# Kernel optimization log

Hardware: AMD Instinct MI355X
Metric: run time of the kernel (lower is better)

The kernel has to match this reference:

```python
import jax, jax.numpy as jnp
import numpy as np

EPS = 1e-5

def _layernorm(x):
    mu = jnp.mean(x, axis=-1, keepdims=True)
    var = jnp.mean((x - mu) ** 2, axis=-1, keepdims=True)
    return (x - mu) / jnp.sqrt(var + EPS)

def _mlp_silu_ln(h, w0, b0, w1, b1):
    z = jnp.maximum(h @ w0 + b0, 0.0) @ w1 + b1
    z = z * jax.nn.sigmoid(z)  # SiLU
    return _layernorm(z)

def _scatter_mean(msgs, tgt, n_nodes):
    s = jax.ops.segment_sum(msgs, tgt, num_segments=n_nodes)
    cnt = jax.ops.segment_sum(jnp.ones((msgs.shape[0],), msgs.dtype), tgt, num_segments=n_nodes)
    return jnp.where(cnt[:, None] > 0, s / jnp.maximum(cnt, 1.0)[:, None], 0.0)

def setup_inputs() -> dict:
    key = jax.random.key(0)
    ks = jax.random.split(key, 6)
    N, E, D_IN, D = 100000, 600000, 64, 128
    s = 0.1
    return {
        "x": jax.random.normal(ks[0], (N, D_IN), jnp.float32),
        "edge_index": jax.random.randint(ks[1], (2, E), 0, N, jnp.int64),
        "ie_w0": jax.random.normal(ks[2], (D_IN, D), jnp.float32) * s,
        "ie_b0": jnp.zeros((D,), jnp.float32),
        "ie_w1": jax.random.normal(ks[3], (D, D), jnp.float32) * s,
        "ie_b1": jnp.zeros((D,), jnp.float32),
        "lw0": jax.random.normal(ks[4], (3, D, D), jnp.float32) * s,
        "lb0": jnp.zeros((3, D), jnp.float32),
        "lw1": jax.random.normal(ks[5], (3, D, D), jnp.float32) * s,
        "lb1": jnp.zeros((3, D), jnp.float32),
    }

def reference(x, edge_index, ie_w0, ie_b0, ie_w1, ie_b1, lw0, lb0, lw1, lb1):
    n_nodes = x.shape[0]
    src, tgt = edge_index[0], edge_index[1]
    # initial embedding: MLP(relu) -> SiLU -> LayerNorm
    h = _mlp_silu_ln(x, ie_w0, ie_b0, ie_w1, ie_b1)

    def step(h, params):
        w0, b0, w1, b1 = params
        z = _mlp_silu_ln(h, w0, b0, w1, b1)
        agg = _scatter_mean(z[src], tgt, n_nodes)  # mean aggregation over incoming edges
        return agg + h, None  # residual

    h, _ = jax.lax.scan(step, h, (lw0, lb0, lw1, lb1))
    return h
```

## Files before the change

kernel.cpp:

```cpp
#include <hip/hip_runtime.h>

typedef short short8 __attribute__((ext_vector_type(8)));
typedef float f32x4 __attribute__((ext_vector_type(4)));

union V16 { uint4 u; unsigned short s[8]; short8 v; };

#define CAP 48

__device__ __forceinline__ unsigned short f2bf(float f) {
  unsigned u = __builtin_bit_cast(unsigned, f);
  u += 0x7fffu + ((u >> 16) & 1u);
  return (unsigned short)(u >> 16);
}
__device__ __forceinline__ float bf2f(unsigned short b) {
  unsigned u = ((unsigned)b) << 16;
  return __builtin_bit_cast(float, u);
}
__device__ __forceinline__ unsigned cvtpk(float lo, float hi) {
  unsigned r;
  asm("v_cvt_pk_bf16_f32 %0, %1, %2" : "=v"(r) : "v"(lo), "v"(hi));
  return r;
}

__device__ __forceinline__ void tcast_one(const float* __restrict__ w,
                                          uint4* __restrict__ wf, int K, int idx) {
  int NF64 = (K / 4) * 64;
  int b = idx / NF64;
  int r = idx - b * NF64;
  int f = r >> 6;
  int l = r & 63;
  int KB = K / 32;
  int n0 = f / KB;
  int k0 = f - n0 * KB;
  int n = n0 * 16 + (l & 15);
  int ks = k0 * 32 + (l >> 4) * 8;
  const float* src = w + (size_t)b * K * 128 + (size_t)ks * 128 + n;
  V16 o;
#pragma unroll
  for (int j = 0; j < 8; j++) o.s[j] = f2bf(src[j * 128]);
  wf[idx] = o.u;
}

__global__ __launch_bounds__(512) void prep_kernel(
    const float* __restrict__ ie_w0, uint4* __restrict__ w0f_ie,
    const float* __restrict__ ie_w1, uint4* __restrict__ w1f_ie,
    const float* __restrict__ lw0, uint4* __restrict__ w0f_l,
    const float* __restrict__ lw1, uint4* __restrict__ w1f_l,
    uint4* __restrict__ cursor4, int nc4,
    const int* __restrict__ ei, int samples, int* __restrict__ flag) {
  int t = blockIdx.x * 512 + threadIdx.x;
  if (t < 1024) { tcast_one(ie_w0, w0f_ie, 64, t); return; }
  t -= 1024;
  if (t < 2048) { tcast_one(ie_w1, w1f_ie, 128, t); return; }
  t -= 2048;
  if (t < 6144) { tcast_one(lw0, w0f_l, 128, t); return; }
  t -= 6144;
  if (t < 6144) { tcast_one(lw1, w1f_l, 128, t); return; }
  t -= 6144;
  if (t < nc4) { uint4 z; z.x = 0; z.y = 0; z.z = 0; z.w = 0; cursor4[t] = z; return; }
  t -= nc4;
  if (t < samples && (t & 1) && ei[t] != 0) atomicOr(flag, 1);
}

__global__ void fill_kernel(const int* __restrict__ ei, const int* __restrict__ flag,
                            int* __restrict__ cursor, int* __restrict__ elist, int E) {
  int e = blockIdx.x * 256 + threadIdx.x;
  if (e >= E) return;
  int f = *flag;
  int s = f ? ei[e] : ei[(size_t)e * 2];
  int t = f ? ei[(size_t)E + e] : ei[((size_t)E + e) * 2];
  int p = atomicAdd(&cursor[t], 1);
  if (p < CAP) elist[t * CAP + p] = s;
}

template <int K, bool OUTBF>
__device__ __forceinline__ void mlp_body(
    const float* __restrict__ in, const uint4* __restrict__ w0f,
    const float* __restrict__ b0, const uint4* __restrict__ w1f,
    const float* __restrict__ b1, float* __restrict__ outF,
    unsigned short* __restrict__ outB, int N, int ntiles,
    uint4* wl, float* bl, int tid) {
  constexpr int KB = K / 32;
  constexpr int NF0 = KB * 8;
  constexpr int TOT = (NF0 + 32) * 64;
  const int lane = tid & 63, wv = tid >> 6;

#pragma unroll
  for (int k = 0; k < TOT / 512; k++) {
    const int i = tid + k * 512;
    const uint4* src = (i < NF0 * 64) ? (w0f + i) : (w1f + (i - NF0 * 64));
    __builtin_amdgcn_global_load_lds(
        (const __attribute__((address_space(1))) void*)src,
        (__attribute__((address_space(3))) void*)(wl + (wv * 64 + k * 512)),
        16, 0, 0);
  }
  if (tid < 128) { bl[tid] = b0[tid]; bl[128 + tid] = b1[tid]; }
  __syncthreads();

  const int c = lane & 15;
  const int q = lane >> 4;
  const int sA = c + 32 * (q & 1);

  for (int tile = blockIdx.x; tile < ntiles; tile += gridDim.x) {
    const int r = tile * 128 + wv * 16 + c;

    short8 afr[KB];
    if (r < N) {
      const float* rp = in + (size_t)r * K + q * 8;
#pragma unroll
      for (int k0 = 0; k0 < KB; k0++) {
        float4 a = *(const float4*)(rp + k0 * 32);
        float4 b = *(const float4*)(rp + k0 * 32 + 4);
        V16 o;
        o.u.x = cvtpk(a.x, a.y); o.u.y = cvtpk(a.z, a.w);
        o.u.z = cvtpk(b.x, b.y); o.u.w = cvtpk(b.z, b.w);
        afr[k0] = o.v;
      }
    } else {
#pragma unroll
      for (int k0 = 0; k0 < KB; k0++) {
        V16 o; o.u.x = 0; o.u.y = 0; o.u.z = 0; o.u.w = 0; afr[k0] = o.v;
      }
    }

    f32x4 acc[8];
#pragma unroll
    for (int n0 = 0; n0 < 8; n0++) {
      acc[n0] = (f32x4){0.f, 0.f, 0.f, 0.f};
#pragma unroll
      for (int k0 = 0; k0 < KB; k0++) {
        V16 w; w.u = wl[(n0 * KB + k0) * 64 + lane];
        acc[n0] = __builtin_amdgcn_mfma_f32_16x16x32_bf16(w.v, afr[k0], acc[n0], 0, 0, 0);
      }
    }

    unsigned pk[8][2];
#pragma unroll
    for (int n0 = 0; n0 < 8; n0++) {
      f32x4 bb = *(const f32x4*)&bl[n0 * 16 + 4 * q];
      float t0 = acc[n0][0] + bb[0]; t0 = t0 > 0.f ? t0 : 0.f;
      float t1 = acc[n0][1] + bb[1]; t1 = t1 > 0.f ? t1 : 0.f;
      float t2 = acc[n0][2] + bb[2]; t2 = t2 > 0.f ? t2 : 0.f;
      float t3 = acc[n0][3] + bb[3]; t3 = t3 > 0.f ? t3 : 0.f;
      pk[n0][0] = cvtpk(t0, t1);
      pk[n0][1] = cvtpk(t2, t3);
    }

    short8 b2[4];
#pragma unroll
    for (int k0 = 0; k0 < 4; k0++) {
      V16 t;
#pragma unroll
      for (int p = 0; p < 4; p++) {
        int src = sA + 16 * (p >> 1);
        unsigned lo = __shfl(pk[2 * k0][p & 1], src, 64);
        unsigned hi = __shfl(pk[2 * k0 + 1][p & 1], src, 64);
        (&t.u.x)[p] = (q & 2) ? hi : lo;
      }
      b2[k0] = t.v;
    }

    f32x4 z[8];
#pragma unroll
    for (int n0 = 0; n0 < 8; n0++) {
      z[n0] = (f32x4){0.f, 0.f, 0.f, 0.f};
#pragma unroll
      for (int k0 = 0; k0 < 4; k0++) {
        V16 w; w.u = wl[NF0 * 64 + (n0 * 4 + k0) * 64 + lane];
        z[n0] = __builtin_amdgcn_mfma_f32_16x16x32_bf16(w.v, b2[k0], z[n0], 0, 0, 0);
      }
    }

    float sum = 0.f, sq = 0.f;
#pragma unroll
    for (int n0 = 0; n0 < 8; n0++) {
      f32x4 bb = *(const f32x4*)&bl[128 + n0 * 16 + 4 * q];
#pragma unroll
      for (int j = 0; j < 4; j++) {
        float v = z[n0][j] + bb[j];
        float sg = v / (1.f + __expf(-v));
        z[n0][j] = sg;
        sum += sg;
        sq += sg * sg;
      }
    }
    sum += __shfl_xor(sum, 16, 64);
    sum += __shfl_xor(sum, 32, 64);
    sq += __shfl_xor(sq, 16, 64);
    sq += __shfl_xor(sq, 32, 64);
    float mu = sum * (1.f / 128.f);
    float rs = rsqrtf(sq * (1.f / 128.f) - mu * mu + 1e-5f);

    if (r < N) {
#pragma unroll
      for (int n0 = 0; n0 < 8; n0++) {
        float v0 = (z[n0][0] - mu) * rs, v1 = (z[n0][1] - mu) * rs;
        float v2 = (z[n0][2] - mu) * rs, v3 = (z[n0][3] - mu) * rs;
        size_t o = (size_t)r * 128 + n0 * 16 + 4 * q;
        if (OUTBF) {
          uint2 st; st.x = cvtpk(v0, v1); st.y = cvtpk(v2, v3);
          *(uint2*)(outB + o) = st;
        } else {
          float4 st; st.x = v0; st.y = v1; st.z = v2; st.w = v3;
          *(float4*)(outF + o) = st;
        }
      }
    }
  }
}

__global__ __launch_bounds__(512, 4) void mlp64_kernel(
    const float* __restrict__ x, const uint4* __restrict__ w0f,
    const float* __restrict__ b0, const uint4* __restrict__ w1f,
    const float* __restrict__ b1, float* __restrict__ h0, int N, int ntiles) {
  __shared__ uint4 wl[48 * 64];
  __shared__ float bl[256];
  mlp_body<64, false>(x, w0f, b0, w1f, b1, h0, nullptr, N, ntiles,
                      wl, bl, threadIdx.x);
}

__global__ __launch_bounds__(512, 4) void mlp128_kernel(
    const float* __restrict__ in, const uint4* __restrict__ w0f,
    const float* __restrict__ b0, const uint4* __restrict__ w1f,
    const float* __restrict__ b1, unsigned short* __restrict__ outB,
    int N, int ntiles) {
  __shared__ uint4 wl[64 * 64];
  __shared__ float bl[256];
  mlp_body<128, true>(in, w0f, b0, w1f, b1, nullptr, outB, N, ntiles,
                      wl, bl, threadIdx.x);
}

__global__ __launch_bounds__(256) void gather_kernel(
    const unsigned short* __restrict__ z, const int* __restrict__ elist,
    const int* __restrict__ cursor, float* __restrict__ h, int N) {
  int t = blockIdx.x * 256 + threadIdx.x;
  int g = t >> 4;
  if (g >= N) return;
  int lane = threadIdx.x & 63;
  int gb = lane & 48;
  int sub = lane & 15;
  int c = sub * 8;
  int o = g * CAP;
  int n = cursor[g];
  n = n < CAP ? n : CAP;
  float* hp = h + (size_t)g * 128 + c;
  float4 h0 = *(const float4*)hp, h1 = *(const float4*)(hp + 4);
  float acc[8] = {0.f, 0.f, 0.f, 0.f, 0.f, 0.f, 0.f, 0.f};
  for (int base = 0; base < n; base += 16) {
    int m = n - base;
    m = m < 16 ? m : 16;
    int sidx = (sub < m) ? elist[o + base + sub] : 0;
    int i = 0;
    for (; i + 4 <= m; i += 4) {
      int s0 = __shfl(sidx, gb + i, 64);
      int s1 = __shfl(sidx, gb + i + 1, 64);
      int s2 = __shfl(sidx, gb + i + 2, 64);
      int s3 = __shfl(sidx, gb + i + 3, 64);
      V16 v0, v1, v2, v3;
      v0.u = *(const uint4*)(z + (size_t)s0 * 128 + c);
      v1.u = *(const uint4*)(z + (size_t)s1 * 128 + c);
      v2.u = *(const uint4*)(z + (size_t)s2 * 128 + c);
      v3.u = *(const uint4*)(z + (size_t)s3 * 128 + c);
#pragma unroll
      for (int j = 0; j < 8; j++)
        acc[j] += (bf2f(v0.s[j]) + bf2f(v1.s[j])) + (bf2f(v2.s[j]) + bf2f(v3.s[j]));
    }
    for (; i < m; i++) {
      int s0 = __shfl(sidx, gb + i, 64);
      V16 v0;
      v0.u = *(const uint4*)(z + (size_t)s0 * 128 + c);
#pragma unroll
      for (int j = 0; j < 8; j++) acc[j] += bf2f(v0.s[j]);
    }
  }
  float inv = n > 0 ? 1.f / (float)n : 0.f;
  h0.x += acc[0] * inv; h0.y += acc[1] * inv; h0.z += acc[2] * inv; h0.w += acc[3] * inv;
  h1.x += acc[4] * inv; h1.y += acc[5] * inv; h1.z += acc[6] * inv; h1.w += acc[7] * inv;
  *(float4*)hp = h0;
  *(float4*)(hp + 4) = h1;
}

extern "C" void kernel_launch(void* const* d_in, const int* in_sizes, int n_in,
                              void* d_out, int out_size, void* d_ws, size_t ws_size,
                              hipStream_t stream) {
  const float* x = (const float*)d_in[0];
  const int* ei = (const int*)d_in[1];
  const float* ie_w0 = (const float*)d_in[2];
  const float* ie_b0 = (const float*)d_in[3];
  const float* ie_w1 = (const float*)d_in[4];
  const float* ie_b1 = (const float*)d_in[5];
  const float* lw0 = (const float*)d_in[6];
  const float* lb0 = (const float*)d_in[7];
  const float* lw1 = (const float*)d_in[8];
  const float* lb1 = (const float*)d_in[9];
  const int N = in_sizes[0] / 64;
  const int E = in_sizes[1] / 2;
  float* h = (float*)d_out;

  char* ws = (char*)d_ws;
  size_t off_b = 0;
  auto carve = [&](size_t bytes) { void* p = ws + off_b; off_b = (off_b + bytes + 255) & ~(size_t)255; return p; };
  unsigned short* zbuf = (unsigned short*)carve((size_t)N * 128 * 2);
  int* elist = (int*)carve((size_t)N * CAP * 4);
  int* flag = (int*)carve(256);
  int* cursor = (int*)carve((size_t)N * 4 + 16);
  uint4* w0f_ie = (uint4*)carve(16 * 64 * 16);
  uint4* w1f_ie = (uint4*)carve(32 * 64 * 16);
  uint4* w0f_l = (uint4*)carve(3 * 32 * 64 * 16);
  uint4* w1f_l = (uint4*)carve(3 * 32 * 64 * 16);

  const int ntiles = (N + 127) / 128;
  const int mgrid = ntiles < 512 ? ntiles : 512;
  const int nc4 = (N + 3) / 4;
  int samples = 2 * E < 8192 ? 2 * E : 8192;

  hipMemsetAsync(flag, 0, 4, stream);
  prep_kernel<<<(15360 + nc4 + samples + 511) / 512, 512, 0, stream>>>(
      ie_w0, w0f_ie, ie_w1, w1f_ie, lw0, w0f_l, lw1, w1f_l,
      (uint4*)cursor, nc4, ei, samples, flag);

  fill_kernel<<<(E + 255) / 256, 256, 0, stream>>>(ei, flag, cursor, elist, E);

  mlp64_kernel<<<mgrid, 512, 0, stream>>>(
      x, w0f_ie, ie_b0, w1f_ie, ie_b1, h, N, ntiles);

  for (int l = 0; l < 3; l++) {
    mlp128_kernel<<<mgrid, 512, 0, stream>>>(
        h, w0f_l + (size_t)l * 32 * 64, lb0 + (size_t)l * 128,
        w1f_l + (size_t)l * 32 * 64, lb1 + (size_t)l * 128, zbuf, N, ntiles);
    gather_kernel<<<((size_t)N * 16 + 255) / 256, 256, 0, stream>>>(
        zbuf, elist, cursor, h, N);
  }
}
```

Measured before the change: 252.4 us.

## Fuse gather-mean residual update with next layer MLP into one kernel

Adds a gmlp kernel that performs the mean aggregation plus residual for layer l, writes h, and immediately runs layer l+1's MLP on the updated row held in registers. The z buffer is now double-buffered so reads and writes can happen in the same kernel. This removes two kernel launches and one round trip of h through global memory per fused layer. In exchange each of the 16 lanes per row handles a whole row's gather serially inside the 512-thread MLP tiling, so there is less parallelism for hiding the latency of the irregular gather loads.

```diff
diff --git a/kernel.cpp b/kernel.cpp
--- a/kernel.cpp
+++ b/kernel.cpp
@@ -74,6 +74,117 @@
 }
 
 template <int K, bool OUTBF>
+__device__ __forceinline__ void mlp_core(
+    const short8 afr[K / 32], const uint4* wl, const float* bl,
+    float* __restrict__ outF, unsigned short* __restrict__ outB,
+    int r, int N, int lane) {
+  constexpr int KB = K / 32;
+  constexpr int NF0 = KB * 8;
+  const int q = lane >> 4;
+  const int c = lane & 15;
+  const int sA = c + 32 * (q & 1);
+
+  f32x4 acc[8];
+#pragma unroll
+  for (int n0 = 0; n0 < 8; n0++) {
+    acc[n0] = (f32x4){0.f, 0.f, 0.f, 0.f};
+#pragma unroll
+    for (int k0 = 0; k0 < KB; k0++) {
+      V16 w; w.u = wl[(n0 * KB + k0) * 64 + lane];
+      acc[n0] = __builtin_amdgcn_mfma_f32_16x16x32_bf16(w.v, afr[k0], acc[n0], 0, 0, 0);
+    }
+  }
+
+  unsigned pk[8][2];
+#pragma unroll
+  for (int n0 = 0; n0 < 8; n0++) {
+    f32x4 bb = *(const f32x4*)&bl[n0 * 16 + 4 * q];
+    float t0 = acc[n0][0] + bb[0]; t0 = t0 > 0.f ? t0 : 0.f;
+    float t1 = acc[n0][1] + bb[1]; t1 = t1 > 0.f ? t1 : 0.f;
+    float t2 = acc[n0][2] + bb[2]; t2 = t2 > 0.f ? t2 : 0.f;
+    float t3 = acc[n0][3] + bb[3]; t3 = t3 > 0.f ? t3 : 0.f;
+    pk[n0][0] = cvtpk(t0, t1);
+    pk[n0][1] = cvtpk(t2, t3);
+  }
+
+  short8 b2[4];
+#pragma unroll
+  for (int k0 = 0; k0 < 4; k0++) {
+    V16 t;
+#pragma unroll
+    for (int p = 0; p < 4; p++) {
+      int src = sA + 16 * (p >> 1);
+      unsigned lo = __shfl(pk[2 * k0][p & 1], src, 64);
+      unsigned hi = __shfl(pk[2 * k0 + 1][p & 1], src, 64);
+      (&t.u.x)[p] = (q & 2) ? hi : lo;
+    }
+    b2[k0] = t.v;
+  }
+
+  f32x4 z[8];
+#pragma unroll
+  for (int n0 = 0; n0 < 8; n0++) {
+    z[n0] = (f32x4){0.f, 0.f, 0.f, 0.f};
+#pragma unroll
+    for (int k0 = 0; k0 < 4; k0++) {
+      V16 w; w.u = wl[NF0 * 64 + (n0 * 4 + k0) * 64 + lane];
+      z[n0] = __builtin_amdgcn_mfma_f32_16x16x32_bf16(w.v, b2[k0], z[n0], 0, 0, 0);
+    }
+  }
+
+  float sum = 0.f, sq = 0.f;
+#pragma unroll
+  for (int n0 = 0; n0 < 8; n0++) {
+    f32x4 bb = *(const f32x4*)&bl[128 + n0 * 16 + 4 * q];
+#pragma unroll
+    for (int j = 0; j < 4; j++) {
+      float v = z[n0][j] + bb[j];
+      float sg = v / (1.f + __expf(-v));
+      z[n0][j] = sg;
+      sum += sg;
+      sq += sg * sg;
+    }
+  }
+  sum += __shfl_xor(sum, 16, 64);
+  sum += __shfl_xor(sum, 32, 64);
+  sq += __shfl_xor(sq, 16, 64);
+  sq += __shfl_xor(sq, 32, 64);
+  float mu = sum * (1.f / 128.f);
+  float rs = rsqrtf(sq * (1.f / 128.f) - mu * mu + 1e-5f);
+
+  if (r < N) {
+#pragma unroll
+    for (int n0 = 0; n0 < 8; n0++) {
+      float v0 = (z[n0][0] - mu) * rs, v1 = (z[n0][1] - mu) * rs;
+      float v2 = (z[n0][2] - mu) * rs, v3 = (z[n0][3] - mu) * rs;
+      size_t o = (size_t)r * 128 + n0 * 16 + 4 * q;
+      if (OUTBF) {
+        uint2 st; st.x = cvtpk(v0, v1); st.y = cvtpk(v2, v3);
+        *(uint2*)(outB + o) = st;
+      } else {
+        float4 st; st.x = v0; st.y = v1; st.z = v2; st.w = v3;
+        *(float4*)(outF + o) = st;
+      }
+    }
+  }
+}
+
+template <int TOT, int NF0>
+__device__ __forceinline__ void stage_weights(const uint4* __restrict__ w0f,
+                                              const uint4* __restrict__ w1f,
+                                              uint4* wl, int tid, int wv) {
+#pragma unroll
+  for (int k = 0; k < TOT / 512; k++) {
+    const int i = tid + k * 512;
+    const uint4* src = (i < NF0 * 64) ? (w0f + i) : (w1f + (i - NF0 * 64));
+    __builtin_amdgcn_global_load_lds(
+        (const __attribute__((address_space(1))) void*)src,
+        (__attribute__((address_space(3))) void*)(wl + (wv * 64 + k * 512)),
+        16, 0, 0);
+  }
+}
+
+template <int K, bool OUTBF>
 __device__ __forceinline__ void mlp_body(
     const float* __restrict__ in, const uint4* __restrict__ w0f,
     const float* __restrict__ b0, const uint4* __restrict__ w1f,
@@ -82,28 +193,16 @@
     uint4* wl, float* bl, int tid) {
   constexpr int KB = K / 32;
   constexpr int NF0 = KB * 8;
-  constexpr int TOT = (NF0 + 32) * 64;
   const int lane = tid & 63, wv = tid >> 6;
-
-#pragma unroll
-  for (int k = 0; k < TOT / 512; k++) {
-    const int i = tid + k * 512;
-    const uint4* src = (i < NF0 * 64) ? (w0f + i) : (w1f + (i - NF0 * 64));
-    __builtin_amdgcn_global_load_lds(
-        (const __attribute__((address_space(1))) void*)src,
-        (__attribute__((address_space(3))) void*)(wl + (wv * 64 + k * 512)),
-        16, 0, 0);
-  }
+  stage_weights<(NF0 + 32) * 64, NF0>(w0f, w1f, wl, tid, wv);
   if (tid < 128) { bl[tid] = b0[tid]; bl[128 + tid] = b1[tid]; }
   __syncthreads();
 
   const int c = lane & 15;
   const int q = lane >> 4;
-  const int sA = c + 32 * (q & 1);
 
   for (int tile = blockIdx.x; tile < ntiles; tile += gridDim.x) {
     const int r = tile * 128 + wv * 16 + c;
-
     short8 afr[KB];
     if (r < N) {
       const float* rp = in + (size_t)r * K + q * 8;
@@ -122,90 +221,7 @@
         V16 o; o.u.x = 0; o.u.y = 0; o.u.z = 0; o.u.w = 0; afr[k0] = o.v;
       }
     }
-
-    f32x4 acc[8];
-#pragma unroll
-    for (int n0 = 0; n0 < 8; n0++) {
-      acc[n0] = (f32x4){0.f, 0.f, 0.f, 0.f};
-#pragma unroll
-      for (int k0 = 0; k0 < KB; k0++) {
-        V16 w; w.u = wl[(n0 * KB + k0) * 64 + lane];
-        acc[n0] = __builtin_amdgcn_mfma_f32_16x16x32_bf16(w.v, afr[k0], acc[n0], 0, 0, 0);
-      }
-    }
-
-    unsigned pk[8][2];
-#pragma unroll
-    for (int n0 = 0; n0 < 8; n0++) {
-      f32x4 bb = *(const f32x4*)&bl[n0 * 16 + 4 * q];
-      float t0 = acc[n0][0] + bb[0]; t0 = t0 > 0.f ? t0 : 0.f;
-      float t1 = acc[n0][1] + bb[1]; t1 = t1 > 0.f ? t1 : 0.f;
-      float t2 = acc[n0][2] + bb[2]; t2 = t2 > 0.f ? t2 : 0.f;
-      float t3 = acc[n0][3] + bb[3]; t3 = t3 > 0.f ? t3 : 0.f;
-      pk[n0][0] = cvtpk(t0, t1);
-      pk[n0][1] = cvtpk(t2, t3);
-    }
-
-    short8 b2[4];
-#pragma unroll
-    for (int k0 = 0; k0 < 4; k0++) {
-      V16 t;
-#pragma unroll
-      for (int p = 0; p < 4; p++) {
-        int src = sA + 16 * (p >> 1);
-        unsigned lo = __shfl(pk[2 * k0][p & 1], src, 64);
-        unsigned hi = __shfl(pk[2 * k0 + 1][p & 1], src, 64);
-        (&t.u.x)[p] = (q & 2) ? hi : lo;
-      }
-      b2[k0] = t.v;
-    }
-
-    f32x4 z[8];
-#pragma unroll
-    for (int n0 = 0; n0 < 8; n0++) {
-      z[n0] = (f32x4){0.f, 0.f, 0.f, 0.f};
-#pragma unroll
-      for (int k0 = 0; k0 < 4; k0++) {
-        V16 w; w.u = wl[NF0 * 64 + (n0 * 4 + k0) * 64 + lane];
-        z[n0] = __builtin_amdgcn_mfma_f32_16x16x32_bf16(w.v, b2[k0], z[n0], 0, 0, 0);
-      }
-    }
-
-    float sum = 0.f, sq = 0.f;
-#pragma unroll
-    for (int n0 = 0; n0 < 8; n0++) {
-      f32x4 bb = *(const f32x4*)&bl[128 + n0 * 16 + 4 * q];
-#pragma unroll
-      for (int j = 0; j < 4; j++) {
-        float v = z[n0][j] + bb[j];
-        float sg = v / (1.f + __expf(-v));
-        z[n0][j] = sg;
-        sum += sg;
-        sq += sg * sg;
-      }
-    }
-    sum += __shfl_xor(sum, 16, 64);
-    sum += __shfl_xor(sum, 32, 64);
-    sq += __shfl_xor(sq, 16, 64);
-    sq += __shfl_xor(sq, 32, 64);
-    float mu = sum * (1.f / 128.f);
-    float rs = rsqrtf(sq * (1.f / 128.f) - mu * mu + 1e-5f);
-
-    if (r < N) {
-#pragma unroll
-      for (int n0 = 0; n0 < 8; n0++) {
-        float v0 = (z[n0][0] - mu) * rs, v1 = (z[n0][1] - mu) * rs;
-        float v2 = (z[n0][2] - mu) * rs, v3 = (z[n0][3] - mu) * rs;
-        size_t o = (size_t)r * 128 + n0 * 16 + 4 * q;
-        if (OUTBF) {
-          uint2 st; st.x = cvtpk(v0, v1); st.y = cvtpk(v2, v3);
-          *(uint2*)(outB + o) = st;
-        } else {
-          float4 st; st.x = v0; st.y = v1; st.z = v2; st.w = v3;
-          *(float4*)(outF + o) = st;
-        }
-      }
-    }
+    mlp_core<K, OUTBF>(afr, wl, bl, outF, outB, r, N, lane);
   }
 }
 
@@ -228,6 +244,107 @@
   __shared__ float bl[256];
   mlp_body<128, true>(in, w0f, b0, w1f, b1, nullptr, outB, N, ntiles,
                       wl, bl, threadIdx.x);
+}
+
+__global__ __launch_bounds__(512) void gmlp_kernel(
+    const unsigned short* __restrict__ zin, const int* __restrict__ elist,
+    const int* __restrict__ cursor, float* __restrict__ h,
+    const uint4* __restrict__ w0f, const float* __restrict__ b0,
+    const uint4* __restrict__ w1f, const float* __restrict__ b1,
+    unsigned short* __restrict__ zout, int N, int ntiles) {
+  __shared__ uint4 wl[64 * 64];
+  __shared__ float bl[256];
+  const int tid = threadIdx.x, lane = tid & 63, wv = tid >> 6;
+  stage_weights<64 * 64, 32>(w0f, w1f, wl, tid, wv);
+  if (tid < 128) { bl[tid] = b0[tid]; bl[128 + tid] = b1[tid]; }
+  __syncthreads();
+
+  const int c = lane & 15;
+  const int q = lane >> 4;
+
+  for (int tile = blockIdx.x; tile < ntiles; tile += gridDim.x) {
+    const int r = tile * 128 + wv * 16 + c;
+    float hv[4][8];
+    if (r < N) {
+      const float* hp = h + (size_t)r * 128 + q * 8;
+      float4 ha[4], hb[4];
+#pragma unroll
+      for (int k0 = 0; k0 < 4; k0++) {
+        ha[k0] = *(const float4*)(hp + k0 * 32);
+        hb[k0] = *(const float4*)(hp + k0 * 32 + 4);
+      }
+      int n = cursor[r];
+      n = n < CAP ? n : CAP;
+      const int o = r * CAP;
+      float acc[4][8];
+#pragma unroll
+      for (int k0 = 0; k0 < 4; k0++)
+#pragma unroll
+        for (int j = 0; j < 8; j++) acc[k0][j] = 0.f;
+      const unsigned short* zq = zin + q * 8;
+      int i = 0;
+      for (; i + 2 <= n; i += 2) {
+        int s0 = elist[o + i], s1 = elist[o + i + 1];
+        V16 u0[4], u1[4];
+#pragma unroll
+        for (int k0 = 0; k0 < 4; k0++) {
+          u0[k0].u = *(const uint4*)(zq + (size_t)s0 * 128 + k0 * 32);
+          u1[k0].u = *(const uint4*)(zq + (size_t)s1 * 128 + k0 * 32);
+        }
+#pragma unroll
+        for (int k0 = 0; k0 < 4; k0++)
+#pragma unroll
+          for (int j = 0; j < 8; j++)
+            acc[k0][j] += bf2f(u0[k0].s[j]) + bf2f(u1[k0].s[j]);
+      }
+      if (i < n) {
+        int s0 = elist[o + i];
+        V16 u0[4];
+#pragma unroll
+        for (int k0 = 0; k0 < 4; k0++)
+          u0[k0].u = *(const uint4*)(zq + (size_t)s0 * 128 + k0 * 32);
+#pragma unroll
+        for (int k0 = 0; k0 < 4; k0++)
+#pragma unroll
+          for (int j = 0; j < 8; j++) acc[k0][j] += bf2f(u0[k0].s[j]);
+      }
+      float inv = n > 0 ? 1.f / (float)n : 0.f;
+      float* hw = h + (size_t)r * 128 + q * 8;
+#pragma unroll
+      for (int k0 = 0; k0 < 4; k0++) {
+        hv[k0][0] = ha[k0].x + acc[k0][0] * inv;
+        hv[k0][1] = ha[k0].y + acc[k0][1] * inv;
+        hv[k0][2] = ha[k0].z + acc[k0][2] * inv;
+        hv[k0][3] = ha[k0].w + acc[k0][3] * inv;
+        hv[k0][4] = hb[k0].x + acc[k0][4] * inv;
+        hv[k0][5] = hb[k0].y + acc[k0][5] * inv;
+        hv[k0][6] = hb[k0].z + acc[k0][6] * inv;
+        hv[k0][7] = hb[k0].w + acc[k0][7] * inv;
+        float4 s0, s1;
+        s0.x = hv[k0][0]; s0.y = hv[k0][1]; s0.z = hv[k0][2]; s0.w = hv[k0][3];
+        s1.x = hv[k0][4]; s1.y = hv[k0][5]; s1.z = hv[k0][6]; s1.w = hv[k0][7];
+        *(float4*)(hw + k0 * 32) = s0;
+        *(float4*)(hw + k0 * 32 + 4) = s1;
+      }
+    } else {
+#pragma unroll
+      for (int k0 = 0; k0 < 4; k0++)
+#pragma unroll
+        for (int j = 0; j < 8; j++) hv[k0][j] = 0.f;
+    }
+
+    short8 afr[4];
+#pragma unroll
+    for (int k0 = 0; k0 < 4; k0++) {
+      V16 o;
+      o.u.x = cvtpk(hv[k0][0], hv[k0][1]);
+      o.u.y = cvtpk(hv[k0][2], hv[k0][3]);
+      o.u.z = cvtpk(hv[k0][4], hv[k0][5]);
+      o.u.w = cvtpk(hv[k0][6], hv[k0][7]);
+      afr[k0] = o.v;
+    }
+    mlp_core<128, true>(afr, wl, bl, nullptr, zout, r, N, lane);
+  }
 }
 
 __global__ __launch_bounds__(256) void gather_kernel(
@@ -300,7 +417,8 @@
   char* ws = (char*)d_ws;
   size_t off_b = 0;
   auto carve = [&](size_t bytes) { void* p = ws + off_b; off_b = (off_b + bytes + 255) & ~(size_t)255; return p; };
-  unsigned short* zbuf = (unsigned short*)carve((size_t)N * 128 * 2);
+  unsigned short* zbufA = (unsigned short*)carve((size_t)N * 128 * 2);
+  unsigned short* zbufB = (unsigned short*)carve((size_t)N * 128 * 2);
   int* elist = (int*)carve((size_t)N * CAP * 4);
   int* flag = (int*)carve(256);
   int* cursor = (int*)carve((size_t)N * 4 + 16);
@@ -324,11 +442,19 @@
   mlp64_kernel<<<mgrid, 512, 0, stream>>>(
       x, w0f_ie, ie_b0, w1f_ie, ie_b1, h, N, ntiles);
 
-  for (int l = 0; l < 3; l++) {
-    mlp128_kernel<<<mgrid, 512, 0, stream>>>(
-        h, w0f_l + (size_t)l * 32 * 64, lb0 + (size_t)l * 128,
-        w1f_l + (size_t)l * 32 * 64, lb1 + (size_t)l * 128, zbuf, N, ntiles);
-    gather_kernel<<<((size_t)N * 16 + 255) / 256, 256, 0, stream>>>(
-        zbuf, elist, cursor, h, N);
-  }
-}
+  mlp128_kernel<<<mgrid, 512, 0, stream>>>(
+      h, w0f_l, lb0, w1f_l, lb1, zbufA, N, ntiles);
+
+  gmlp_kernel<<<mgrid, 512, 0, stream>>>(
+      zbufA, elist, cursor, h,
+      w0f_l + (size_t)1 * 32 * 64, lb0 + 128,
+      w1f_l + (size_t)1 * 32 * 64, lb1 + 128, zbufB, N, ntiles);
+
+  gmlp_kernel<<<mgrid, 512, 0, stream>>>(
+      zbufB, elist, cursor, h,
+      w0f_l + (size_t)2 * 32 * 64, lb0 + 256,
+      w1f_l + (size_t)2 * 32 * 64, lb1 + 256, zbufA, N, ntiles);
+
+  gather_kernel<<<((size_t)N * 16 + 255) / 256, 256, 0, stream>>>(
+      zbufA, elist, cursor, h, N);
+}
```

Measured after the change: 257.5 us. 2.1% more time.

## Fuse initial embedding MLP with first layer MLP in one kernel

Applied to the files above, without the earlier changes.

Merges the input-embedding MLP and the layer-0 MLP into a single kernel. Each block handles two tiles, keeps the embedding output in registers as bf16 MFMA fragments, then restages layer-0 weights in shared memory and computes z0 directly. This drops one kernel launch and avoids reading h back from global memory for layer 0. In exchange it uses more registers (launch bounds no longer request 4 blocks per CU), adds an extra weight staging pass per block, and rounds h to bf16 before layer 0, as the old kernel already did when it reloaded h.

```diff
diff --git a/kernel.cpp b/kernel.cpp
--- a/kernel.cpp
+++ b/kernel.cpp
@@ -73,18 +73,97 @@
   if (p < CAP) elist[t * CAP + p] = s;
 }
 
-template <int K, bool OUTBF>
-__device__ __forceinline__ void mlp_body(
-    const float* __restrict__ in, const uint4* __restrict__ w0f,
-    const float* __restrict__ b0, const uint4* __restrict__ w1f,
-    const float* __restrict__ b1, float* __restrict__ outF,
-    unsigned short* __restrict__ outB, int N, int ntiles,
-    uint4* wl, float* bl, int tid) {
+__device__ __forceinline__ void make_bfrags(const unsigned pk[8][2], int lane,
+                                            short8 b2[4]) {
+  const int q = lane >> 4;
+  const int c = lane & 15;
+  const int sA = c + 32 * (q & 1);
+#pragma unroll
+  for (int k0 = 0; k0 < 4; k0++) {
+    V16 t;
+#pragma unroll
+    for (int p = 0; p < 4; p++) {
+      int src = sA + 16 * (p >> 1);
+      unsigned lo = __shfl(pk[2 * k0][p & 1], src, 64);
+      unsigned hi = __shfl(pk[2 * k0 + 1][p & 1], src, 64);
+      (&t.u.x)[p] = (q & 2) ? hi : lo;
+    }
+    b2[k0] = t.v;
+  }
+}
+
+template <int K>
+__device__ __forceinline__ void mlp_compute(
+    const short8* afr, const uint4* wl, const float* bl, int lane, f32x4 z[8]) {
   constexpr int KB = K / 32;
   constexpr int NF0 = KB * 8;
-  constexpr int TOT = (NF0 + 32) * 64;
-  const int lane = tid & 63, wv = tid >> 6;
-
+  const int q = lane >> 4;
+
+  f32x4 acc[8];
+#pragma unroll
+  for (int n0 = 0; n0 < 8; n0++) {
+    acc[n0] = (f32x4){0.f, 0.f, 0.f, 0.f};
+#pragma unroll
+    for (int k0 = 0; k0 < KB; k0++) {
+      V16 w; w.u = wl[(n0 * KB + k0) * 64 + lane];
+      acc[n0] = __builtin_amdgcn_mfma_f32_16x16x32_bf16(w.v, afr[k0], acc[n0], 0, 0, 0);
+    }
+  }
+
+  unsigned pk[8][2];
+#pragma unroll
+  for (int n0 = 0; n0 < 8; n0++) {
+    f32x4 bb = *(const f32x4*)&bl[n0 * 16 + 4 * q];
+    float t0 = acc[n0][0] + bb[0]; t0 = t0 > 0.f ? t0 : 0.f;
+    float t1 = acc[n0][1] + bb[1]; t1 = t1 > 0.f ? t1 : 0.f;
+    float t2 = acc[n0][2] + bb[2]; t2 = t2 > 0.f ? t2 : 0.f;
+    float t3 = acc[n0][3] + bb[3]; t3 = t3 > 0.f ? t3 : 0.f;
+    pk[n0][0] = cvtpk(t0, t1);
+    pk[n0][1] = cvtpk(t2, t3);
+  }
+
+  short8 b2[4];
+  make_bfrags(pk, lane, b2);
+
+#pragma unroll
+  for (int n0 = 0; n0 < 8; n0++) {
+    z[n0] = (f32x4){0.f, 0.f, 0.f, 0.f};
+#pragma unroll
+    for (int k0 = 0; k0 < 4; k0++) {
+      V16 w; w.u = wl[NF0 * 64 + (n0 * 4 + k0) * 64 + lane];
+      z[n0] = __builtin_amdgcn_mfma_f32_16x16x32_bf16(w.v, b2[k0], z[n0], 0, 0, 0);
+    }
+  }
+
+  float sum = 0.f, sq = 0.f;
+#pragma unroll
+  for (int n0 = 0; n0 < 8; n0++) {
+    f32x4 bb = *(const f32x4*)&bl[128 + n0 * 16 + 4 * q];
+#pragma unroll
+    for (int j = 0; j < 4; j++) {
+      float v = z[n0][j] + bb[j];
+      float sg = v / (1.f + __expf(-v));
+      z[n0][j] = sg;
+      sum += sg;
+      sq += sg * sg;
+    }
+  }
+  sum += __shfl_xor(sum, 16, 64);
+  sum += __shfl_xor(sum, 32, 64);
+  sq += __shfl_xor(sq, 16, 64);
+  sq += __shfl_xor(sq, 32, 64);
+  float mu = sum * (1.f / 128.f);
+  float rs = rsqrtf(sq * (1.f / 128.f) - mu * mu + 1e-5f);
+#pragma unroll
+  for (int n0 = 0; n0 < 8; n0++)
+#pragma unroll
+    for (int j = 0; j < 4; j++) z[n0][j] = (z[n0][j] - mu) * rs;
+}
+
+template <int TOT, int NF0>
+__device__ __forceinline__ void stage_weights(const uint4* __restrict__ w0f,
+                                              const uint4* __restrict__ w1f,
+                                              uint4* wl, int tid, int wv) {
 #pragma unroll
   for (int k = 0; k < TOT / 512; k++) {
     const int i = tid + k * 512;
@@ -94,129 +173,30 @@
         (__attribute__((address_space(3))) void*)(wl + (wv * 64 + k * 512)),
         16, 0, 0);
   }
-  if (tid < 128) { bl[tid] = b0[tid]; bl[128 + tid] = b1[tid]; }
-  __syncthreads();
-
-  const int c = lane & 15;
+}
+
+template <int K>
+__device__ __forceinline__ void load_afr(const float* __restrict__ in, int r, int N,
+                                         int lane, short8* afr) {
+  constexpr int KB = K / 32;
   const int q = lane >> 4;
-  const int sA = c + 32 * (q & 1);
-
-  for (int tile = blockIdx.x; tile < ntiles; tile += gridDim.x) {
-    const int r = tile * 128 + wv * 16 + c;
-
-    short8 afr[KB];
-    if (r < N) {
-      const float* rp = in + (size_t)r * K + q * 8;
-#pragma unroll
-      for (int k0 = 0; k0 < KB; k0++) {
-        float4 a = *(const float4*)(rp + k0 * 32);
-        float4 b = *(const float4*)(rp + k0 * 32 + 4);
-        V16 o;
-        o.u.x = cvtpk(a.x, a.y); o.u.y = cvtpk(a.z, a.w);
-        o.u.z = cvtpk(b.x, b.y); o.u.w = cvtpk(b.z, b.w);
-        afr[k0] = o.v;
-      }
-    } else {
-#pragma unroll
-      for (int k0 = 0; k0 < KB; k0++) {
-        V16 o; o.u.x = 0; o.u.y = 0; o.u.z = 0; o.u.w = 0; afr[k0] = o.v;
-      }
-    }
-
-    f32x4 acc[8];
-#pragma unroll
-    for (int n0 = 0; n0 < 8; n0++) {
-      acc[n0] = (f32x4){0.f, 0.f, 0.f, 0.f};
-#pragma unroll
-      for (int k0 = 0; k0 < KB; k0++) {
-        V16 w; w.u = wl[(n0 * KB + k0) * 64 + lane];
-        acc[n0] = __builtin_amdgcn_mfma_f32_16x16x32_bf16(w.v, afr[k0], acc[n0], 0, 0, 0);
-      }
-    }
-
-    unsigned pk[8][2];
-#pragma unroll
-    for (int n0 = 0; n0 < 8; n0++) {
-      f32x4 bb = *(const f32x4*)&bl[n0 * 16 + 4 * q];
-      float t0 = acc[n0][0] + bb[0]; t0 = t0 > 0.f ? t0 : 0.f;
-      float t1 = acc[n0][1] + bb[1]; t1 = t1 > 0.f ? t1 : 0.f;
-      float t2 = acc[n0][2] + bb[2]; t2 = t2 > 0.f ? t2 : 0.f;
-      float t3 = acc[n0][3] + bb[3]; t3 = t3 > 0.f ? t3 : 0.f;
-      pk[n0][0] = cvtpk(t0, t1);
-      pk[n0][1] = cvtpk(t2, t3);
-    }
-
-    short8 b2[4];
-#pragma unroll
-    for (int k0 = 0; k0 < 4; k0++) {
-      V16 t;
-#pragma unroll
-      for (int p = 0; p < 4; p++) {
-        int src = sA + 16 * (p >> 1);
-        unsigned lo = __shfl(pk[2 * k0][p & 1], src, 64);
-        unsigned hi = __shfl(pk[2 * k0 + 1][p & 1], src, 64);
-        (&t.u.x)[p] = (q & 2) ? hi : lo;
-      }
-      b2[k0] = t.v;
-    }
-
-    f32x4 z[8];
-#pragma unroll
-    for (int n0 = 0; n0 < 8; n0++) {
-      z[n0] = (f32x4){0.f, 0.f, 0.f, 0.f};
-#pragma unroll
-      for (int k0 = 0; k0 < 4; k0++) {
-        V16 w; w.u = wl[NF0 * 64 + (n0 * 4 + k0) * 64 + lane];
-        z[n0] = __builtin_amdgcn_mfma_f32_16x16x32_bf16(w.v, b2[k0], z[n0], 0, 0, 0);
-      }
-    }
-
-    float sum = 0.f, sq = 0.f;
-#pragma unroll
-    for (int n0 = 0; n0 < 8; n0++) {
-      f32x4 bb = *(const f32x4*)&bl[128 + n0 * 16 + 4 * q];
-#pragma unroll
-      for (int j = 0; j < 4; j++) {
-        float v = z[n0][j] + bb[j];
-        float sg = v / (1.f + __expf(-v));
-        z[n0][j] = sg;
-        sum += sg;
-        sq += sg * sg;
-      }
-    }
-    sum += __shfl_xor(sum, 16, 64);
-    sum += __shfl_xor(sum, 32, 64);
-    sq += __shfl_xor(sq, 16, 64);
-    sq += __shfl_xor(sq, 32, 64);
-    float mu = sum * (1.f / 128.f);
-    float rs = rsqrtf(sq * (1.f / 128.f) - mu * mu + 1e-5f);
-
-    if (r < N) {
-#pragma unroll
-      for (int n0 = 0; n0 < 8; n0++) {
-        float v0 = (z[n0][0] - mu) * rs, v1 = (z[n0][1] - mu) * rs;
-        float v2 = (z[n0][2] - mu) * rs, v3 = (z[n0][3] - mu) * rs;
-        size_t o = (size_t)r * 128 + n0 * 16 + 4 * q;
-        if (OUTBF) {
-          uint2 st; st.x = cvtpk(v0, v1); st.y = cvtpk(v2, v3);
-          *(uint2*)(outB + o) = st;
-        } else {
-          float4 st; st.x = v0; st.y = v1; st.z = v2; st.w = v3;
-          *(float4*)(outF + o) = st;
-        }
-      }
-    }
-  }
-}
-
-__global__ __launch_bounds__(512, 4) void mlp64_kernel(
-    const float* __restrict__ x, const uint4* __restrict__ w0f,
-    const float* __restrict__ b0, const uint4* __restrict__ w1f,
-    const float* __restrict__ b1, float* __restrict__ h0, int N, int ntiles) {
-  __shared__ uint4 wl[48 * 64];
-  __shared__ float bl[256];
-  mlp_body<64, false>(x, w0f, b0, w1f, b1, h0, nullptr, N, ntiles,
-                      wl, bl, threadIdx.x);
+  if (r < N) {
+    const float* rp = in + (size_t)r * K + q * 8;
+#pragma unroll
+    for (int k0 = 0; k0 < KB; k0++) {
+      float4 a = *(const float4*)(rp + k0 * 32);
+      float4 b = *(const float4*)(rp + k0 * 32 + 4);
+      V16 o;
+      o.u.x = cvtpk(a.x, a.y); o.u.y = cvtpk(a.z, a.w);
+      o.u.z = cvtpk(b.x, b.y); o.u.w = cvtpk(b.z, b.w);
+      afr[k0] = o.v;
+    }
+  } else {
+#pragma unroll
+    for (int k0 = 0; k0 < KB; k0++) {
+      V16 o; o.u.x = 0; o.u.y = 0; o.u.z = 0; o.u.w = 0; afr[k0] = o.v;
+    }
+  }
 }
 
 __global__ __launch_bounds__(512, 4) void mlp128_kernel(
@@ -226,8 +206,101 @@
     int N, int ntiles) {
   __shared__ uint4 wl[64 * 64];
   __shared__ float bl[256];
-  mlp_body<128, true>(in, w0f, b0, w1f, b1, nullptr, outB, N, ntiles,
-                      wl, bl, threadIdx.x);
+  const int tid = threadIdx.x, lane = tid & 63, wv = tid >> 6;
+  stage_weights<64 * 64, 32>(w0f, w1f, wl, tid, wv);
+  if (tid < 128) { bl[tid] = b0[tid]; bl[128 + tid] = b1[tid]; }
+  __syncthreads();
+
+  const int c = lane & 15;
+  const int q = lane >> 4;
+  for (int tile = blockIdx.x; tile < ntiles; tile += gridDim.x) {
+    const int r = tile * 128 + wv * 16 + c;
+    short8 afr[4];
+    load_afr<128>(in, r, N, lane, afr);
+    f32x4 z[8];
+    mlp_compute<128>(afr, wl, bl, lane, z);
+    if (r < N) {
+#pragma unroll
+      for (int n0 = 0; n0 < 8; n0++) {
+        uint2 st;
+        st.x = cvtpk(z[n0][0], z[n0][1]);
+        st.y = cvtpk(z[n0][2], z[n0][3]);
+        *(uint2*)(outB + (size_t)r * 128 + n0 * 16 + 4 * q) = st;
+      }
+    }
+  }
+}
+
+__global__ __launch_bounds__(512) void mlp2_kernel(
+    const float* __restrict__ x,
+    const uint4* __restrict__ w0f_ie, const float* __restrict__ b0i,
+    const uint4* __restrict__ w1f_ie, const float* __restrict__ b1i,
+    const uint4* __restrict__ w0f_l, const float* __restrict__ b0l,
+    const uint4* __restrict__ w1f_l, const float* __restrict__ b1l,
+    float* __restrict__ h0, unsigned short* __restrict__ z0,
+    int N, int ntiles) {
+  __shared__ uint4 wl[64 * 64];
+  __shared__ float bl[512];
+  const int tid = threadIdx.x, lane = tid & 63, wv = tid >> 6;
+  stage_weights<48 * 64, 16>(w0f_ie, w1f_ie, wl, tid, wv);
+  if (tid < 128) {
+    bl[tid] = b0i[tid]; bl[128 + tid] = b1i[tid];
+    bl[256 + tid] = b0l[tid]; bl[384 + tid] = b1l[tid];
+  }
+  __syncthreads();
+
+  const int c = lane & 15;
+  const int q = lane >> 4;
+
+  short8 fsave[2][4];
+
+#pragma unroll
+  for (int t = 0; t < 2; t++) {
+    const int tile = blockIdx.x + t * gridDim.x;
+    if (tile >= ntiles) break;
+    const int r = tile * 128 + wv * 16 + c;
+    short8 afr[2];
+    load_afr<64>(x, r, N, lane, afr);
+    f32x4 z[8];
+    mlp_compute<64>(afr, wl, bl, lane, z);
+    if (r < N) {
+      float* hw = h0 + (size_t)r * 128 + q * 4;
+#pragma unroll
+      for (int n0 = 0; n0 < 8; n0++) {
+        float4 st; st.x = z[n0][0]; st.y = z[n0][1]; st.z = z[n0][2]; st.w = z[n0][3];
+        *(float4*)(hw + n0 * 16) = st;
+      }
+    }
+    unsigned pk[8][2];
+#pragma unroll
+    for (int n0 = 0; n0 < 8; n0++) {
+      pk[n0][0] = cvtpk(z[n0][0], z[n0][1]);
+      pk[n0][1] = cvtpk(z[n0][2], z[n0][3]);
+    }
+    make_bfrags(pk, lane, fsave[t]);
+  }
+  __syncthreads();
+
+  stage_weights<64 * 64, 32>(w0f_l, w1f_l, wl, tid, wv);
+  __syncthreads();
+
+#pragma unroll
+  for (int t = 0; t < 2; t++) {
+    const int tile = blockIdx.x + t * gridDim.x;
+    if (tile >= ntiles) break;
+    const int r = tile * 128 + wv * 16 + c;
+    f32x4 z[8];
+    mlp_compute<128>(fsave[t], wl, bl + 256, lane, z);
+    if (r < N) {
+#pragma unroll
+      for (int n0 = 0; n0 < 8; n0++) {
+        uint2 st;
+        st.x = cvtpk(z[n0][0], z[n0][1]);
+        st.y = cvtpk(z[n0][2], z[n0][3]);
+        *(uint2*)(z0 + (size_t)r * 128 + n0 * 16 + 4 * q) = st;
+      }
+    }
+  }
 }
 
 __global__ __launch_bounds__(256) void gather_kernel(
@@ -311,6 +384,7 @@
 
   const int ntiles = (N + 127) / 128;
   const int mgrid = ntiles < 512 ? ntiles : 512;
+  const int mgrid2 = (ntiles + 1) / 2;
   const int nc4 = (N + 3) / 4;
   int samples = 2 * E < 8192 ? 2 * E : 8192;
 
@@ -321,10 +395,13 @@
 
   fill_kernel<<<(E + 255) / 256, 256, 0, stream>>>(ei, flag, cursor, elist, E);
 
-  mlp64_kernel<<<mgrid, 512, 0, stream>>>(
-      x, w0f_ie, ie_b0, w1f_ie, ie_b1, h, N, ntiles);
-
-  for (int l = 0; l < 3; l++) {
+  mlp2_kernel<<<mgrid2, 512, 0, stream>>>(
+      x, w0f_ie, ie_b0, w1f_ie, ie_b1,
+      w0f_l, lb0, w1f_l, lb1, h, zbuf, N, ntiles);
+  gather_kernel<<<((size_t)N * 16 + 255) / 256, 256, 0, stream>>>(
+      zbuf, elist, cursor, h, N);
+
+  for (int l = 1; l < 3; l++) {
     mlp128_kernel<<<mgrid, 512, 0, stream>>>(
         h, w0f_l + (size_t)l * 32 * 64, lb0 + (size_t)l * 128,
         w1f_l + (size_t)l * 32 * 64, lb1 + (size_t)l * 128, zbuf, N, ntiles);
```

Result: faster. 246.3 us, median of 2 (-2.4%).
